# Optimization experiments

Hardware: AMD Instinct MI355X
Metric: run time of the kernel (lower is better)

## Reference

```python
import jax, jax.numpy as jnp
import numpy as np

C, N, G = 10, 500000, 8


def setup_inputs() -> dict:
    key = jax.random.key(0)
    k1, k2 = jax.random.split(key)
    group_act = jax.random.uniform(k1, (C, N, G), dtype=jnp.float32)
    target_labels = jax.random.randint(k2, (N,), 0, 11, dtype=jnp.int64 if jax.config.jax_enable_x64 else jnp.int32)
    return {"group_act": group_act, "target_labels": target_labels}


def reference(group_act, target_labels):
    # group_act: [C, N, G] (stacked list_group_activation), target_labels: [N] in 0..C (0 => ignored)
    labels = target_labels.reshape(-1) - 1                      # [N], -1 => skip
    c, n, g = group_act.shape
    masks = (labels[None, :] == jnp.arange(c)[:, None]).astype(group_act.dtype)  # [C, N]
    counts = masks.sum(axis=1)                                  # [C]
    valid = counts >= 2                                         # classes actually contributing

    Am = group_act * masks[:, :, None]                          # [C, N, G] masked activations
    col_sum = Am.sum(axis=1)                                    # [C, G]
    p = Am / col_sum[:, None, :]                                # normalized per column (zero on unmasked rows)
    # log only over masked rows (original indexes rows by cls_mask before log)
    m3 = masks[:, :, None] > 0
    logp = jnp.where(m3, jnp.log(jnp.where(m3, p, 1.0)), 0.0)   # [C, N, G]

    # M[c, i, j] = sum_n p[c,n,i] * log p[c,n,j]; loss_ij = -M[c,i,j] for i != j
    M = jnp.einsum('cni,cnj->cij', p, logp)                     # [C, G, G]
    offdiag = M * (1.0 - jnp.eye(g, dtype=M.dtype))
    per_class = offdiag.sum(axis=(1, 2))                        # [C]

    num = jnp.sum(jnp.where(valid, per_class, 0.0))
    denom = jnp.sum(valid.astype(M.dtype)) * (g * (g - 1))
    # original: tot = mean(-M_ij); return -tot == mean(M_ij)
    return num / denom
```

## Files before the change

### kernel.cpp

```cpp
#include <hip/hip_runtime.h>

#define C_CLS 10
#define G_DIM 8
#define CHUNKS 128
#define ACC_W 25
#define NBLK (CHUNKS * C_CLS)
#define NSTRIPE 16
#define NTOT (C_CLS * ACC_W)

__device__ inline float wave_red(float v) {
#pragma unroll
    for (int off = 32; off > 0; off >>= 1) v += __shfl_down(v, off, 64);
    return v;
}

__global__ void __launch_bounds__(256) k_main(const float* __restrict__ ga,
                                              const int* __restrict__ lbl,
                                              float* __restrict__ acc,
                                              unsigned int* __restrict__ ticket,
                                              float* __restrict__ out, int N) {
    const int c = blockIdx.y;
    const int cc = c + 1;
    const int chunk_len = (((N + CHUNKS - 1) / CHUNKS) + 3) & ~3;
    const int base = blockIdx.x * chunk_len;
    const int end = min(base + chunk_len, N);

    float cs_a[G_DIM] = {0,0,0,0,0,0,0,0};
    float R_a[G_DIM]  = {0,0,0,0,0,0,0,0};
    float D_a[G_DIM]  = {0,0,0,0,0,0,0,0};
    float cnt = 0.0f;

    const float* plane = ga + (size_t)c * N * G_DIM;

    for (int n4 = base + (int)threadIdx.x * 4; n4 < end; n4 += 256 * 4) {
        int l[4];
        if (n4 + 3 < end) {
            const int4 lv = *(const int4*)(lbl + n4);
            l[0] = lv.x; l[1] = lv.y; l[2] = lv.z; l[3] = lv.w;
        } else {
            for (int k = 0; k < 4; ++k) l[k] = (n4 + k < end) ? lbl[n4 + k] : 0;
        }
#pragma unroll
        for (int k = 0; k < 4; ++k) {
            const int n = n4 + k;
            if (n < end && l[k] == cc) {
                const float4* row = (const float4*)(plane + (size_t)n * G_DIM);
                const float4 v0 = row[0];
                const float4 v1 = row[1];
                float a[G_DIM] = {v0.x, v0.y, v0.z, v0.w, v1.x, v1.y, v1.z, v1.w};
                float la[G_DIM], L = 0.0f;
#pragma unroll
                for (int g = 0; g < G_DIM; ++g) {
                    la[g] = __logf(fmaxf(a[g], 1e-30f));
                    L += la[g];
                }
                cnt += 1.0f;
#pragma unroll
                for (int g = 0; g < G_DIM; ++g) {
                    cs_a[g] += a[g];
                    R_a[g] = fmaf(a[g], L, R_a[g]);
                    D_a[g] = fmaf(a[g], la[g], D_a[g]);
                }
            }
        }
    }

#pragma unroll
    for (int g = 0; g < G_DIM; ++g) {
        cs_a[g] = wave_red(cs_a[g]);
        R_a[g]  = wave_red(R_a[g]);
        D_a[g]  = wave_red(D_a[g]);
    }
    cnt = wave_red(cnt);

    __shared__ float s_part[4][ACC_W];
    const int wid = threadIdx.x >> 6, lid = threadIdx.x & 63;
    if (lid == 0) {
#pragma unroll
        for (int g = 0; g < G_DIM; ++g) {
            s_part[wid][g]      = cs_a[g];
            s_part[wid][8 + g]  = R_a[g];
            s_part[wid][16 + g] = D_a[g];
        }
        s_part[wid][24] = cnt;
    }
    __syncthreads();
    const int t = threadIdx.x;
    const int stripe = blockIdx.x & (NSTRIPE - 1);
    if (t < ACC_W) {
        float v = s_part[0][t] + s_part[1][t] + s_part[2][t] + s_part[3][t];
        atomicAdd(&acc[stripe * NTOT + c * ACC_W + t], v);
    }

    asm volatile("s_waitcnt vmcnt(0)" ::: "memory");
    __syncthreads();
    __shared__ unsigned int s_rank;
    if (t == 0) s_rank = atomicAdd(ticket, 1u);
    __syncthreads();
    if (s_rank != NBLK - 1) return;

    __shared__ float s_acc[NTOT];
    if (t < NTOT) {
        float s = 0.0f;
#pragma unroll
        for (int st = 0; st < NSTRIPE; ++st)
            s += atomicAdd(&acc[st * NTOT + t], 0.0f);
        s_acc[t] = s;
    }
    __syncthreads();
    if (t == 0) {
        float tot = 0.0f;
        int nv = 0;
        for (int fc = 0; fc < C_CLS; ++fc) {
            const float* sa = s_acc + fc * ACC_W;
            if (sa[24] >= 2.0f) {
                nv++;
                float K = 0.0f, ss = 0.0f;
                for (int i = 0; i < G_DIM; ++i) {
                    float cs = sa[i];
                    K += __logf(cs);
                    ss += (sa[8 + i] - sa[16 + i]) / cs;
                }
                tot += ss - (float)(G_DIM - 1) * K;
            }
        }
        out[0] = tot / ((float)nv * (float)(G_DIM * (G_DIM - 1)));
    }
}

extern "C" void kernel_launch(void* const* d_in, const int* in_sizes, int n_in,
                              void* d_out, int out_size, void* d_ws, size_t ws_size,
                              hipStream_t stream) {
    const float* ga = (const float*)d_in[0];
    const int* lbl = (const int*)d_in[1];
    float* out = (float*)d_out;
    const int N = in_sizes[1];

    float* acc = (float*)d_ws;
    unsigned int* ticket =
        (unsigned int*)((unsigned char*)d_ws + NSTRIPE * NTOT * sizeof(float));

    hipMemsetAsync(d_ws, 0, NSTRIPE * NTOT * sizeof(float) + sizeof(unsigned int),
                   stream);

    dim3 grid(CHUNKS, C_CLS);
    k_main<<<grid, 256, 0, stream>>>(ga, lbl, acc, ticket, out, N);
}
```

Before: 227.9 us.

## Replace atomic ticket reduction with per-block partials and a finalize kernel

The main kernel now writes per-block partial sums to a workspace array instead of striped atomics followed by a last-block ticket. A separate single-block kernel reduces those partials and computes the loss, which removes the memset and the atomic tail. The inner loop also handles 8 labels per thread per iteration instead of 4, so it issues more independent loads per pass. The cost is one extra kernel launch.

```diff
diff --git a/kernel.cpp b/kernel.cpp
--- a/kernel.cpp
+++ b/kernel.cpp
@@ -4,8 +4,6 @@
 #define G_DIM 8
 #define CHUNKS 128
 #define ACC_W 25
-#define NBLK (CHUNKS * C_CLS)
-#define NSTRIPE 16
 #define NTOT (C_CLS * ACC_W)
 
 __device__ inline float wave_red(float v) {
@@ -16,12 +14,10 @@
 
 __global__ void __launch_bounds__(256) k_main(const float* __restrict__ ga,
                                               const int* __restrict__ lbl,
-                                              float* __restrict__ acc,
-                                              unsigned int* __restrict__ ticket,
-                                              float* __restrict__ out, int N) {
+                                              float* __restrict__ part, int N) {
     const int c = blockIdx.y;
     const int cc = c + 1;
-    const int chunk_len = (((N + CHUNKS - 1) / CHUNKS) + 3) & ~3;
+    const int chunk_len = (((N + CHUNKS - 1) / CHUNKS) + 7) & ~7;
     const int base = blockIdx.x * chunk_len;
     const int end = min(base + chunk_len, N);
 
@@ -32,19 +28,22 @@
 
     const float* plane = ga + (size_t)c * N * G_DIM;
 
-    for (int n4 = base + (int)threadIdx.x * 4; n4 < end; n4 += 256 * 4) {
-        int l[4];
-        if (n4 + 3 < end) {
-            const int4 lv = *(const int4*)(lbl + n4);
-            l[0] = lv.x; l[1] = lv.y; l[2] = lv.z; l[3] = lv.w;
+    for (int n8 = base + (int)threadIdx.x * 8; n8 < end; n8 += 256 * 8) {
+        int l[8];
+        if (n8 + 7 < end) {
+            const int4 lv0 = *(const int4*)(lbl + n8);
+            const int4 lv1 = *(const int4*)(lbl + n8 + 4);
+            l[0] = lv0.x; l[1] = lv0.y; l[2] = lv0.z; l[3] = lv0.w;
+            l[4] = lv1.x; l[5] = lv1.y; l[6] = lv1.z; l[7] = lv1.w;
         } else {
-            for (int k = 0; k < 4; ++k) l[k] = (n4 + k < end) ? lbl[n4 + k] : 0;
+#pragma unroll
+            for (int k = 0; k < 8; ++k)
+                l[k] = (n8 + k < end) ? lbl[n8 + k] : 0;
         }
 #pragma unroll
-        for (int k = 0; k < 4; ++k) {
-            const int n = n4 + k;
-            if (n < end && l[k] == cc) {
-                const float4* row = (const float4*)(plane + (size_t)n * G_DIM);
+        for (int k = 0; k < 8; ++k) {
+            if (l[k] == cc) {
+                const float4* row = (const float4*)(plane + (size_t)(n8 + k) * G_DIM);
                 const float4 v0 = row[0];
                 const float4 v1 = row[1];
                 float a[G_DIM] = {v0.x, v0.y, v0.z, v0.w, v1.x, v1.y, v1.z, v1.w};
@@ -86,33 +85,36 @@
     }
     __syncthreads();
     const int t = threadIdx.x;
-    const int stripe = blockIdx.x & (NSTRIPE - 1);
     if (t < ACC_W) {
         float v = s_part[0][t] + s_part[1][t] + s_part[2][t] + s_part[3][t];
-        atomicAdd(&acc[stripe * NTOT + c * ACC_W + t], v);
+        part[((size_t)(c * ACC_W + t)) * CHUNKS + blockIdx.x] = v;
     }
+}
 
-    asm volatile("s_waitcnt vmcnt(0)" ::: "memory");
-    __syncthreads();
-    __shared__ unsigned int s_rank;
-    if (t == 0) s_rank = atomicAdd(ticket, 1u);
-    __syncthreads();
-    if (s_rank != NBLK - 1) return;
-
+__global__ void __launch_bounds__(512) k_fin(const float* __restrict__ part,
+                                             float* __restrict__ out) {
+    __shared__ float s_half[NTOT][2];
     __shared__ float s_acc[NTOT];
-    if (t < NTOT) {
+    const int t = threadIdx.x;
+    if (t < NTOT * 2) {
+        const int a = t >> 1, h = t & 1;
+        const float4* p = (const float4*)(part + (size_t)a * CHUNKS + h * (CHUNKS / 2));
         float s = 0.0f;
 #pragma unroll
-        for (int st = 0; st < NSTRIPE; ++st)
-            s += atomicAdd(&acc[st * NTOT + t], 0.0f);
-        s_acc[t] = s;
+        for (int i = 0; i < CHUNKS / 8; ++i) {
+            const float4 v = p[i];
+            s += (v.x + v.y) + (v.z + v.w);
+        }
+        s_half[a][h] = s;
     }
+    __syncthreads();
+    if (t < NTOT) s_acc[t] = s_half[t][0] + s_half[t][1];
     __syncthreads();
     if (t == 0) {
         float tot = 0.0f;
         int nv = 0;
-        for (int fc = 0; fc < C_CLS; ++fc) {
-            const float* sa = s_acc + fc * ACC_W;
+        for (int c = 0; c < C_CLS; ++c) {
+            const float* sa = s_acc + c * ACC_W;
             if (sa[24] >= 2.0f) {
                 nv++;
                 float K = 0.0f, ss = 0.0f;
@@ -136,13 +138,9 @@
     float* out = (float*)d_out;
     const int N = in_sizes[1];
 
-    float* acc = (float*)d_ws;
-    unsigned int* ticket =
-        (unsigned int*)((unsigned char*)d_ws + NSTRIPE * NTOT * sizeof(float));
-
-    hipMemsetAsync(d_ws, 0, NSTRIPE * NTOT * sizeof(float) + sizeof(unsigned int),
-                   stream);
+    float* part = (float*)d_ws;
 
     dim3 grid(CHUNKS, C_CLS);
-    k_main<<<grid, 256, 0, stream>>>(ga, lbl, acc, ticket, out, N);
+    k_main<<<grid, 256, 0, stream>>>(ga, lbl, part, N);
+    k_fin<<<1, 512, 0, stream>>>(part, out);
 }
```

Result: faster. 219.6 us (median of 2 runs) (-3.6%).
